# Kernel optimization log

Hardware: AMD Instinct MI355X
Metric: run time of the kernel (lower is better)

## Reference

```python
import jax, jax.numpy as jnp
import numpy as np

B, S, D, H = 2, 2048, 1024, 16
HD = D // H  # head_dim = 64
NEG = -1.0e9


def setup_inputs() -> dict:
    key = jax.random.key(0)
    ks = jax.random.split(key, 9)
    s = 1.0 / np.sqrt(D)
    return {
        "x": jax.random.normal(ks[0], (B, S, D), jnp.float32),
        "mask": jnp.ones((B, S), jnp.float32),
        "Wq": jax.random.normal(ks[1], (D, D), jnp.float32) * s,
        "bq": jnp.zeros((D,), jnp.float32),
        "Wk": jax.random.normal(ks[2], (D, D), jnp.float32) * s,
        "bk": jnp.zeros((D,), jnp.float32),
        "Wv": jax.random.normal(ks[3], (D, D), jnp.float32) * s,
        "bv": jnp.zeros((D,), jnp.float32),
        "Wo": jax.random.normal(ks[4], (D, D), jnp.float32) * s,
        "bo": jnp.zeros((D,), jnp.float32),
    }


def reference(x, mask, Wq, bq, Wk, bk, Wv, bv, Wo, bo):
    # QKV projections -> [B, H, S, HD]
    def proj(t, W, b):
        return (t @ W + b).reshape(B, S, H, HD).transpose(0, 2, 1, 3)

    q = proj(x, Wq, bq)
    k = proj(x, Wk, bk)
    v = proj(x, Wv, bv)

    scores = jnp.einsum("bhqd,bhkd->bhqk", q, k) / jnp.sqrt(jnp.asarray(HD, x.dtype))
    # causal mask: scores * m + (1-m) * -1e9 (matches original exactly)
    cm = jnp.tril(jnp.ones((S, S), x.dtype))[None, None]
    scores = scores * cm + (1.0 - cm) * NEG
    # 2D padding mask branch
    scores = scores + (1.0 - mask[:, None, None, :]) * NEG

    attn = jax.nn.softmax(scores, axis=-1)
    out = jnp.einsum("bhqk,bhkd->bqhd", attn, v).reshape(B, S, D)
    return out @ Wo + bo
```

## Files before the change

kernel.cpp:

```cpp
#include <hip/hip_runtime.h>
#include <cstdint>
#include <cstddef>

typedef __attribute__((ext_vector_type(8))) short short8;
typedef __attribute__((ext_vector_type(4))) float floatx4;
typedef __attribute__((ext_vector_type(4))) unsigned short ushortx4;
typedef __attribute__((ext_vector_type(4))) unsigned int uintx4;

#define MFMA16(a, b, c) __builtin_amdgcn_mfma_f32_16x16x32_bf16((a), (b), (c), 0, 0, 0)

__device__ __forceinline__ unsigned short f2bf(float f) {
  unsigned int u = __builtin_bit_cast(unsigned int, f);
  u += 0x7fffu + ((u >> 16) & 1u);
  return (unsigned short)(u >> 16);
}

typedef __attribute__((address_space(1))) void gvoid_t;
typedef __attribute__((address_space(3))) void svoid_t;
__device__ __forceinline__ void gload_lds16(const void* g, void* l) {
  __builtin_amdgcn_global_load_lds((gvoid_t*)(uintptr_t)g, (svoid_t*)(uintptr_t)l, 16, 0, 0);
}

__global__ void convert_x(const float* __restrict__ x, unsigned short* __restrict__ xb) {
  int i = (blockIdx.x * 256 + threadIdx.x) * 4;
  floatx4 v = *(const floatx4*)(x + i);
  ushortx4 o;
  o[0] = f2bf(v[0]); o[1] = f2bf(v[1]); o[2] = f2bf(v[2]); o[3] = f2bf(v[3]);
  *(ushortx4*)(xb + i) = o;
}

__global__ void transpose_w(const float* __restrict__ Wq, const float* __restrict__ Wk,
                            const float* __restrict__ Wv, const float* __restrict__ Wo,
                            unsigned short* __restrict__ Wqkvt, unsigned short* __restrict__ Wot) {
  __shared__ float tile[32][33];
  int z = blockIdx.z;
  const float* W = (z == 0) ? Wq : (z == 1) ? Wk : (z == 2) ? Wv : Wo;
  unsigned short* out = (z == 3) ? Wot : (Wqkvt + (size_t)z * 1024 * 1024);
  int n0 = blockIdx.x * 32, k0 = blockIdx.y * 32;
  int tx = threadIdx.x, ty = threadIdx.y;
#pragma unroll
  for (int j = 0; j < 4; ++j)
    tile[ty + j * 8][tx] = W[(size_t)(k0 + ty + j * 8) * 1024 + n0 + tx];
  __syncthreads();
#pragma unroll
  for (int j = 0; j < 4; ++j)
    out[(size_t)(n0 + ty + j * 8) * 1024 + k0 + tx] = f2bf(tile[tx][ty + j * 8]);
}

#define GEMM_PROLOGUE()                                                        \
  __shared__ __align__(16) unsigned short As[128 * 64];                        \
  __shared__ __align__(16) unsigned short Bs[128 * 64];                        \
  const int tid = threadIdx.x;                                                 \
  const int lane = tid & 63;                                                   \
  const int wid = tid >> 6;                                                    \
  const int col = lane & 15;                                                   \
  const int quad = lane >> 4;                                                  \
  const int m0 = blockIdx.x * 128;                                             \
  const int n0 = blockIdx.y * 128;                                             \
  const int wm = wid >> 1;                                                     \
  const int wn = wid & 1;                                                      \
  floatx4 acc[4][4];                                                           \
  _Pragma("unroll") for (int i = 0; i < 4; ++i)                                \
      _Pragma("unroll") for (int j = 0; j < 4; ++j)                            \
          acc[i][j] = (floatx4)(0.f);                                          \
  _Pragma("unroll 1") for (int kt = 0; kt < 16; ++kt) {                        \
    __syncthreads();                                                           \
    _Pragma("unroll") for (int call = 0; call < 4; ++call) {                   \
      int c = call * 256 + tid;                                                \
      int r = c >> 3, ch = c & 7;                                              \
      int gk = kt * 64 + ((ch ^ (r & 7)) * 8);                                 \
      gload_lds16(A + (size_t)(m0 + r) * 1024 + gk,                            \
                  As + (size_t)(call * 256 + wid * 64) * 8);                   \
      gload_lds16(Bt + (size_t)(n0 + r) * 1024 + gk,                           \
                  Bs + (size_t)(call * 256 + wid * 64) * 8);                   \
    }                                                                          \
    __syncthreads();                                                           \
    _Pragma("unroll") for (int ks = 0; ks < 2; ++ks) {                         \
      short8 af[4], bf[4];                                                     \
      _Pragma("unroll") for (int rt = 0; rt < 4; ++rt) {                       \
        int row = wm * 64 + rt * 16 + col;                                     \
        af[rt] = *(const short8*)&As[row * 64 + (((ks * 4 + quad) ^ (row & 7)) * 8)]; \
      }                                                                        \
      _Pragma("unroll") for (int ct = 0; ct < 4; ++ct) {                       \
        int row = wn * 64 + ct * 16 + col;                                     \
        bf[ct] = *(const short8*)&Bs[row * 64 + (((ks * 4 + quad) ^ (row & 7)) * 8)]; \
      }                                                                        \
      _Pragma("unroll") for (int rt = 0; rt < 4; ++rt)                         \
          _Pragma("unroll") for (int ct = 0; ct < 4; ++ct)                     \
              acc[rt][ct] = MFMA16(af[rt], bf[ct], acc[rt][ct]);               \
    }                                                                          \
  }

__global__ __launch_bounds__(256)
void gemm_qkv(const unsigned short* __restrict__ A, const unsigned short* __restrict__ Bt,
              const float* __restrict__ bq, const float* __restrict__ bk,
              const float* __restrict__ bv,
              unsigned short* __restrict__ Qo, unsigned short* __restrict__ Ko,
              unsigned short* __restrict__ Vo) {
  GEMM_PROLOGUE()
  const int nseg = n0 >> 10;
  const float* bias = (nseg == 0) ? bq : ((nseg == 1) ? bk : bv);
#pragma unroll
  for (int rt = 0; rt < 4; ++rt) {
#pragma unroll
    for (int ct = 0; ct < 4; ++ct) {
      int mg = m0 + wm * 64 + rt * 16 + quad * 4;
      int ng = n0 + wn * 64 + ct * 16 + col;
      int c = ng & 1023;
      int hh = c >> 6, hd = c & 63;
      int b_ = mg >> 11, s = mg & 2047;
      float bb = bias[c];
      if (nseg == 2) {
        ushortx4 pk;
#pragma unroll
        for (int i = 0; i < 4; ++i) pk[i] = f2bf(acc[rt][ct][i] + bb);
        *(ushortx4*)&Vo[(size_t)(b_ * 16 + hh) * 131072 + (size_t)hd * 2048 + s] = pk;
      } else {
        unsigned short* dst =
            ((nseg == 0) ? Qo : Ko) + ((size_t)(b_ * 16 + hh) * 2048 + s) * 64 + hd;
        float scl = (nseg == 0) ? 0.125f : 1.0f;
#pragma unroll
        for (int i = 0; i < 4; ++i) dst[(size_t)i * 64] = f2bf((acc[rt][ct][i] + bb) * scl);
      }
    }
  }
}

__global__ __launch_bounds__(256)
void gemm_out(const unsigned short* __restrict__ A, const unsigned short* __restrict__ Bt,
              const float* __restrict__ bo, float* __restrict__ Out) {
  GEMM_PROLOGUE()
#pragma unroll
  for (int rt = 0; rt < 4; ++rt) {
#pragma unroll
    for (int ct = 0; ct < 4; ++ct) {
      int mg = m0 + wm * 64 + rt * 16 + quad * 4;
      int ng = n0 + wn * 64 + ct * 16 + col;
      float bb = bo[ng];
#pragma unroll
      for (int i = 0; i < 4; ++i)
        Out[(size_t)(mg + i) * 1024 + ng] = acc[rt][ct][i] + bb;
    }
  }
}

__global__ __launch_bounds__(256, 3)
void flash_attn(const unsigned short* __restrict__ Q, const unsigned short* __restrict__ K,
                const unsigned short* __restrict__ Vt, const float* __restrict__ mask,
                unsigned short* __restrict__ O) {
  __shared__ __align__(16) unsigned short Ks[128 * 64];
  __shared__ __align__(16) unsigned short Vs[64 * 128];
  __shared__ __align__(16) unsigned short Ps[64 * 128];

  const int tid = threadIdx.x;
  const int lane = tid & 63;
  const int wid = tid >> 6;
  const int col = lane & 15;
  const int quad = lane >> 4;
  const int j = 31 - (int)(blockIdx.x >> 5);
  const int bh = blockIdx.x & 31;
  const int b = bh >> 4, h = bh & 15;
  const int q0 = j * 64;
  const int tdiag = j >> 1;

  const unsigned short* Qp = Q + (size_t)bh * 2048 * 64;
  const unsigned short* Kp = K + (size_t)bh * 2048 * 64;
  const unsigned short* Vp = Vt + (size_t)bh * 64 * 2048;
  const float* mp = mask + b * 2048;

  const int lr8 = lane >> 3, lc8 = lane & 7;
  const int lr16 = lane >> 4, lc16 = lane & 15;
  const floatx4 fzero = (floatx4)(0.f);
  const floatx4 fone = (floatx4)(1.f);

#pragma unroll
  for (int i = 0; i < 2; ++i) {
    int seg = wid * 2 + i;
    int r = seg * 8 + lr8;
    gload_lds16(Qp + (size_t)(q0 + r) * 64 + ((lc8 ^ (r & 7)) * 8), Ps + seg * 512);
  }
  __syncthreads();
  short8 qf[2];
  {
    int q = wid * 16 + col;
#pragma unroll
    for (int ks = 0; ks < 2; ++ks)
      qf[ks] = *(const short8*)&Ps[q * 64 + (((ks * 4 + quad) ^ (q & 7)) * 8)];
  }

  floatx4 o[4];
#pragma unroll
  for (int dt = 0; dt < 4; ++dt) o[dt] = fzero;
  float mrow = -1e30f;
  float lrow = 0.f;

#pragma unroll 1
  for (int t = 0; t <= tdiag; ++t) {
    if (t > 0) __syncthreads();
#pragma unroll
    for (int i = 0; i < 4; ++i) {
      int seg = wid * 4 + i;
      int r = seg * 8 + lr8;
      gload_lds16(Kp + (size_t)(t * 128 + r) * 64 + ((lc8 ^ (r & 7)) * 8), Ks + seg * 512);
    }
#pragma unroll
    for (int i = 0; i < 4; ++i) {
      int seg = wid * 4 + i;
      int r = seg * 4 + lr16;
      gload_lds16(Vp + (size_t)r * 2048 + t * 128 + ((lc16 ^ (r & 15)) * 8), Vs + seg * 512);
    }
    __syncthreads();

    floatx4 mbias[8];
#pragma unroll
    for (int rt = 0; rt < 8; ++rt) {
      floatx4 mm = *(const floatx4*)&mp[t * 128 + rt * 16 + quad * 4];
      mbias[rt] = (fone - mm) * -1.0e9f;
    }

    floatx4 sc[8];
#pragma unroll
    for (int rt = 0; rt < 8; ++rt) {
      int kr = rt * 16 + col;
      short8 kf0 = *(const short8*)&Ks[kr * 64 + ((quad ^ (col & 7)) * 8)];
      short8 kf1 = *(const short8*)&Ks[kr * 64 + (((4 + quad) ^ (col & 7)) * 8)];
      floatx4 s0 = MFMA16(kf0, qf[0], fzero);
      s0 = MFMA16(kf1, qf[1], s0);
      sc[rt] = s0 + mbias[rt];
    }
    if (t == tdiag) {
      int qg = q0 + wid * 16 + col;
#pragma unroll
      for (int rt = 0; rt < 8; ++rt)
#pragma unroll
        for (int i = 0; i < 4; ++i)
          if (t * 128 + rt * 16 + quad * 4 + i > qg) sc[rt][i] = -1.0e9f;
    }

    float mt = -1e30f;
#pragma unroll
    for (int rt = 0; rt < 8; ++rt)
      mt = fmaxf(mt, fmaxf(fmaxf(sc[rt][0], sc[rt][1]), fmaxf(sc[rt][2], sc[rt][3])));
    mt = fmaxf(mt, __shfl_xor(mt, 16));
    mt = fmaxf(mt, __shfl_xor(mt, 32));
    float mn = fmaxf(mrow, mt);
    float alpha = __expf(mrow - mn);
    mrow = mn;
    float sum = 0.f;
#pragma unroll
    for (int rt = 0; rt < 8; ++rt)
#pragma unroll
      for (int i = 0; i < 4; ++i) {
        float p = __expf(sc[rt][i] - mn);
        sc[rt][i] = p;
        sum += p;
      }
    sum += __shfl_xor(sum, 16);
    sum += __shfl_xor(sum, 32);
    lrow = lrow * alpha + sum;
#pragma unroll
    for (int dt = 0; dt < 4; ++dt) o[dt] *= alpha;
    {
      int qloc = wid * 16 + col;
#pragma unroll
      for (int rt = 0; rt < 8; ++rt) {
        ushortx4 pk;
#pragma unroll
        for (int i = 0; i < 4; ++i) pk[i] = f2bf(sc[rt][i]);
        int chunk = (rt * 2 + (quad >> 1)) ^ col;
        *(ushortx4*)&Ps[qloc * 128 + chunk * 8 + (quad & 1) * 4] = pk;
      }
    }
#pragma unroll
    for (int ks = 0; ks < 4; ++ks) {
      int ch = ks * 4 + quad;
      short8 pf = *(const short8*)&Ps[(wid * 16 + col) * 128 + ((ch ^ col) * 8)];
#pragma unroll
      for (int dt = 0; dt < 4; ++dt) {
        short8 vf = *(const short8*)&Vs[(dt * 16 + col) * 128 + ((ch ^ col) * 8)];
        o[dt] = MFMA16(vf, pf, o[dt]);
      }
    }
  }

  {
    float inv = 1.0f / lrow;
    int qg = q0 + wid * 16 + col;
    unsigned short* dst = O + ((size_t)(b * 2048 + qg)) * 1024 + h * 64;
#pragma unroll
    for (int dt = 0; dt < 4; ++dt) {
      ushortx4 pk;
#pragma unroll
      for (int i = 0; i < 4; ++i) pk[i] = f2bf(o[dt][i] * inv);
      *(ushortx4*)&dst[dt * 16 + quad * 4] = pk;
    }
  }
}

extern "C" void kernel_launch(void* const* d_in, const int* in_sizes, int n_in,
                              void* d_out, int out_size, void* d_ws, size_t ws_size,
                              hipStream_t stream) {
  (void)in_sizes; (void)n_in; (void)out_size; (void)ws_size;
  const float* x  = (const float*)d_in[0];
  const float* mask = (const float*)d_in[1];
  const float* Wq = (const float*)d_in[2];
  const float* bq = (const float*)d_in[3];
  const float* Wk = (const float*)d_in[4];
  const float* bk = (const float*)d_in[5];
  const float* Wv = (const float*)d_in[6];
  const float* bv = (const float*)d_in[7];
  const float* Wo = (const float*)d_in[8];
  const float* bo = (const float*)d_in[9];
  float* out = (float*)d_out;

  char* ws = (char*)d_ws;
  unsigned short* xb    = (unsigned short*)(ws);
  unsigned short* Wqkvt = (unsigned short*)(ws + (8u << 20));
  unsigned short* Wot   = (unsigned short*)(ws + (14u << 20));
  unsigned short* Qb    = (unsigned short*)(ws + (16u << 20));
  unsigned short* Kb    = (unsigned short*)(ws + (24u << 20));
  unsigned short* Vtb   = (unsigned short*)(ws + (32u << 20));
  unsigned short* Ao    = (unsigned short*)(ws + (40u << 20));

  convert_x<<<4096, 256, 0, stream>>>(x, xb);
  transpose_w<<<dim3(32, 32, 4), dim3(32, 8), 0, stream>>>(Wq, Wk, Wv, Wo, Wqkvt, Wot);
  gemm_qkv<<<dim3(32, 24), 256, 0, stream>>>(xb, Wqkvt, bq, bk, bv, Qb, Kb, Vtb);
  flash_attn<<<dim3(1024), 256, 0, stream>>>(Qb, Kb, Vtb, mask, Ao);
  gemm_out<<<dim3(32, 8), 256, 0, stream>>>(Ao, Wot, bo, out);
}
```

Measured before the change: 197.4 us.

## Shrink GEMM M-tile and attention KV tile to 64 for more occupancy

Both GEMMs move from 128x128 to 64x128 block tiles, which doubles the grid so more workgroups run across the CUs; the output GEMM in particular goes from 256 to 512 blocks. The flash attention kernel switches from 128-wide KV tiles to 64-wide tiles that line up with the 64-row query blocks. This removes the wasted causal work on the diagonal tile and shrinks LDS use. The P buffer now uses a padded row stride instead of an XOR swizzle, and launch bounds are raised to 5 waves per SIMD. The trade-off is less data reuse per tile, more loop iterations with their barriers, and tighter register limits.

Result: slower. 204.7 us (+3.7%).

```diff
diff --git a/kernel.cpp b/kernel.cpp
--- a/kernel.cpp
+++ b/kernel.cpp
@@ -5,7 +5,7 @@
 typedef __attribute__((ext_vector_type(8))) short short8;
 typedef __attribute__((ext_vector_type(4))) float floatx4;
 typedef __attribute__((ext_vector_type(4))) unsigned short ushortx4;
-typedef __attribute__((ext_vector_type(4))) unsigned int uintx4;
+typedef __attribute__((ext_vector_type(2))) unsigned int uintx2;
 
 #define MFMA16(a, b, c) __builtin_amdgcn_mfma_f32_16x16x32_bf16((a), (b), (c), 0, 0, 0)
 
@@ -13,6 +13,10 @@
   unsigned int u = __builtin_bit_cast(unsigned int, f);
   u += 0x7fffu + ((u >> 16) & 1u);
   return (unsigned short)(u >> 16);
+}
+
+__device__ __forceinline__ unsigned int pk_bf16(float a, float b) {
+  return (unsigned int)f2bf(a) | ((unsigned int)f2bf(b) << 16);
 }
 
 typedef __attribute__((address_space(1))) void gvoid_t;
@@ -48,50 +52,53 @@
 }
 
 #define GEMM_PROLOGUE()                                                        \
-  __shared__ __align__(16) unsigned short As[128 * 64];                        \
+  __shared__ __align__(16) unsigned short As[64 * 64];                         \
   __shared__ __align__(16) unsigned short Bs[128 * 64];                        \
   const int tid = threadIdx.x;                                                 \
   const int lane = tid & 63;                                                   \
   const int wid = tid >> 6;                                                    \
   const int col = lane & 15;                                                   \
   const int quad = lane >> 4;                                                  \
-  const int m0 = blockIdx.x * 128;                                             \
+  const int m0 = blockIdx.x * 64;                                              \
   const int n0 = blockIdx.y * 128;                                             \
   const int wm = wid >> 1;                                                     \
   const int wn = wid & 1;                                                      \
-  floatx4 acc[4][4];                                                           \
-  _Pragma("unroll") for (int i = 0; i < 4; ++i)                                \
+  floatx4 acc[2][4];                                                           \
+  _Pragma("unroll") for (int i = 0; i < 2; ++i)                                \
       _Pragma("unroll") for (int j = 0; j < 4; ++j)                            \
           acc[i][j] = (floatx4)(0.f);                                          \
   _Pragma("unroll 1") for (int kt = 0; kt < 16; ++kt) {                        \
     __syncthreads();                                                           \
+    _Pragma("unroll") for (int call = 0; call < 2; ++call) {                   \
+      int c = call * 256 + tid;                                                \
+      int r = c >> 3, ch = c & 7;                                              \
+      gload_lds16(A + (size_t)(m0 + r) * 1024 + kt * 64 + ((ch ^ (r & 7)) * 8),\
+                  As + (size_t)(call * 256 + wid * 64) * 8);                   \
+    }                                                                          \
     _Pragma("unroll") for (int call = 0; call < 4; ++call) {                   \
       int c = call * 256 + tid;                                                \
       int r = c >> 3, ch = c & 7;                                              \
-      int gk = kt * 64 + ((ch ^ (r & 7)) * 8);                                 \
-      gload_lds16(A + (size_t)(m0 + r) * 1024 + gk,                            \
-                  As + (size_t)(call * 256 + wid * 64) * 8);                   \
-      gload_lds16(Bt + (size_t)(n0 + r) * 1024 + gk,                           \
+      gload_lds16(Bt + (size_t)(n0 + r) * 1024 + kt * 64 + ((ch ^ (r & 7)) * 8),\
                   Bs + (size_t)(call * 256 + wid * 64) * 8);                   \
     }                                                                          \
     __syncthreads();                                                           \
     _Pragma("unroll") for (int ks = 0; ks < 2; ++ks) {                         \
-      short8 af[4], bf[4];                                                     \
-      _Pragma("unroll") for (int rt = 0; rt < 4; ++rt) {                       \
-        int row = wm * 64 + rt * 16 + col;                                     \
+      short8 af[2], bf[4];                                                     \
+      _Pragma("unroll") for (int rt = 0; rt < 2; ++rt) {                       \
+        int row = wm * 32 + rt * 16 + col;                                     \
         af[rt] = *(const short8*)&As[row * 64 + (((ks * 4 + quad) ^ (row & 7)) * 8)]; \
       }                                                                        \
       _Pragma("unroll") for (int ct = 0; ct < 4; ++ct) {                       \
         int row = wn * 64 + ct * 16 + col;                                     \
         bf[ct] = *(const short8*)&Bs[row * 64 + (((ks * 4 + quad) ^ (row & 7)) * 8)]; \
       }                                                                        \
-      _Pragma("unroll") for (int rt = 0; rt < 4; ++rt)                         \
+      _Pragma("unroll") for (int rt = 0; rt < 2; ++rt)                         \
           _Pragma("unroll") for (int ct = 0; ct < 4; ++ct)                     \
               acc[rt][ct] = MFMA16(af[rt], bf[ct], acc[rt][ct]);               \
     }                                                                          \
   }
 
-__global__ __launch_bounds__(256)
+__global__ __launch_bounds__(256, 5)
 void gemm_qkv(const unsigned short* __restrict__ A, const unsigned short* __restrict__ Bt,
               const float* __restrict__ bq, const float* __restrict__ bk,
               const float* __restrict__ bv,
@@ -101,10 +108,10 @@
   const int nseg = n0 >> 10;
   const float* bias = (nseg == 0) ? bq : ((nseg == 1) ? bk : bv);
 #pragma unroll
-  for (int rt = 0; rt < 4; ++rt) {
+  for (int rt = 0; rt < 2; ++rt) {
 #pragma unroll
     for (int ct = 0; ct < 4; ++ct) {
-      int mg = m0 + wm * 64 + rt * 16 + quad * 4;
+      int mg = m0 + wm * 32 + rt * 16 + quad * 4;
       int ng = n0 + wn * 64 + ct * 16 + col;
       int c = ng & 1023;
       int hh = c >> 6, hd = c & 63;
@@ -126,15 +133,15 @@
   }
 }
 
-__global__ __launch_bounds__(256)
+__global__ __launch_bounds__(256, 5)
 void gemm_out(const unsigned short* __restrict__ A, const unsigned short* __restrict__ Bt,
               const float* __restrict__ bo, float* __restrict__ Out) {
   GEMM_PROLOGUE()
 #pragma unroll
-  for (int rt = 0; rt < 4; ++rt) {
+  for (int rt = 0; rt < 2; ++rt) {
 #pragma unroll
     for (int ct = 0; ct < 4; ++ct) {
-      int mg = m0 + wm * 64 + rt * 16 + quad * 4;
+      int mg = m0 + wm * 32 + rt * 16 + quad * 4;
       int ng = n0 + wn * 64 + ct * 16 + col;
       float bb = bo[ng];
 #pragma unroll
@@ -144,13 +151,13 @@
   }
 }
 
-__global__ __launch_bounds__(256, 3)
+__global__ __launch_bounds__(256, 5)
 void flash_attn(const unsigned short* __restrict__ Q, const unsigned short* __restrict__ K,
                 const unsigned short* __restrict__ Vt, const float* __restrict__ mask,
                 unsigned short* __restrict__ O) {
-  __shared__ __align__(16) unsigned short Ks[128 * 64];
-  __shared__ __align__(16) unsigned short Vs[64 * 128];
-  __shared__ __align__(16) unsigned short Ps[64 * 128];
+  __shared__ __align__(16) unsigned short Ks[64 * 64];
+  __shared__ __align__(16) unsigned short Vs[64 * 64];
+  __shared__ __align__(16) unsigned short Ps[64 * 72];
 
   const int tid = threadIdx.x;
   const int lane = tid & 63;
@@ -161,23 +168,21 @@
   const int bh = blockIdx.x & 31;
   const int b = bh >> 4, h = bh & 15;
   const int q0 = j * 64;
-  const int tdiag = j >> 1;
+  const int C = j + 1;
 
   const unsigned short* Qp = Q + (size_t)bh * 2048 * 64;
   const unsigned short* Kp = K + (size_t)bh * 2048 * 64;
   const unsigned short* Vp = Vt + (size_t)bh * 64 * 2048;
   const float* mp = mask + b * 2048;
-
-  const int lr8 = lane >> 3, lc8 = lane & 7;
-  const int lr16 = lane >> 4, lc16 = lane & 15;
   const floatx4 fzero = (floatx4)(0.f);
   const floatx4 fone = (floatx4)(1.f);
 
 #pragma unroll
   for (int i = 0; i < 2; ++i) {
-    int seg = wid * 2 + i;
-    int r = seg * 8 + lr8;
-    gload_lds16(Qp + (size_t)(q0 + r) * 64 + ((lc8 ^ (r & 7)) * 8), Ps + seg * 512);
+    int c = i * 256 + tid;
+    int r = c >> 3, ch = c & 7;
+    gload_lds16(Qp + (size_t)(q0 + r) * 64 + ((ch ^ (r & 7)) * 8),
+                Ps + (size_t)(i * 256 + wid * 64) * 8);
   }
   __syncthreads();
   short8 qf[2];
@@ -195,51 +200,54 @@
   float lrow = 0.f;
 
 #pragma unroll 1
-  for (int t = 0; t <= tdiag; ++t) {
+  for (int t = 0; t < C; ++t) {
+    const int kv0 = t * 64;
     if (t > 0) __syncthreads();
 #pragma unroll
-    for (int i = 0; i < 4; ++i) {
-      int seg = wid * 4 + i;
-      int r = seg * 8 + lr8;
-      gload_lds16(Kp + (size_t)(t * 128 + r) * 64 + ((lc8 ^ (r & 7)) * 8), Ks + seg * 512);
-    }
-#pragma unroll
-    for (int i = 0; i < 4; ++i) {
-      int seg = wid * 4 + i;
-      int r = seg * 4 + lr16;
-      gload_lds16(Vp + (size_t)r * 2048 + t * 128 + ((lc16 ^ (r & 15)) * 8), Vs + seg * 512);
+    for (int i = 0; i < 2; ++i) {
+      int c = i * 256 + tid;
+      int r = c >> 3, ch = c & 7;
+      gload_lds16(Kp + (size_t)(kv0 + r) * 64 + ((ch ^ (r & 7)) * 8),
+                  Ks + (size_t)(i * 256 + wid * 64) * 8);
+    }
+#pragma unroll
+    for (int i = 0; i < 2; ++i) {
+      int c = i * 256 + tid;
+      int r = c >> 3, ch = c & 7;
+      gload_lds16(Vp + (size_t)r * 2048 + kv0 + ((ch ^ (r & 7)) * 8),
+                  Vs + (size_t)(i * 256 + wid * 64) * 8);
     }
     __syncthreads();
 
-    floatx4 mbias[8];
-#pragma unroll
-    for (int rt = 0; rt < 8; ++rt) {
-      floatx4 mm = *(const floatx4*)&mp[t * 128 + rt * 16 + quad * 4];
+    floatx4 mbias[4];
+#pragma unroll
+    for (int rt = 0; rt < 4; ++rt) {
+      floatx4 mm = *(const floatx4*)&mp[kv0 + rt * 16 + quad * 4];
       mbias[rt] = (fone - mm) * -1.0e9f;
     }
 
-    floatx4 sc[8];
-#pragma unroll
-    for (int rt = 0; rt < 8; ++rt) {
+    floatx4 sc[4];
+#pragma unroll
+    for (int rt = 0; rt < 4; ++rt) {
       int kr = rt * 16 + col;
-      short8 kf0 = *(const short8*)&Ks[kr * 64 + ((quad ^ (col & 7)) * 8)];
-      short8 kf1 = *(const short8*)&Ks[kr * 64 + (((4 + quad) ^ (col & 7)) * 8)];
+      short8 kf0 = *(const short8*)&Ks[kr * 64 + ((quad ^ (kr & 7)) * 8)];
+      short8 kf1 = *(const short8*)&Ks[kr * 64 + (((4 + quad) ^ (kr & 7)) * 8)];
       floatx4 s0 = MFMA16(kf0, qf[0], fzero);
       s0 = MFMA16(kf1, qf[1], s0);
       sc[rt] = s0 + mbias[rt];
     }
-    if (t == tdiag) {
+    if (t == C - 1) {
       int qg = q0 + wid * 16 + col;
 #pragma unroll
-      for (int rt = 0; rt < 8; ++rt)
+      for (int rt = 0; rt < 4; ++rt)
 #pragma unroll
         for (int i = 0; i < 4; ++i)
-          if (t * 128 + rt * 16 + quad * 4 + i > qg) sc[rt][i] = -1.0e9f;
+          if (kv0 + rt * 16 + quad * 4 + i > qg) sc[rt][i] = -1.0e9f;
     }
 
     float mt = -1e30f;
 #pragma unroll
-    for (int rt = 0; rt < 8; ++rt)
+    for (int rt = 0; rt < 4; ++rt)
       mt = fmaxf(mt, fmaxf(fmaxf(sc[rt][0], sc[rt][1]), fmaxf(sc[rt][2], sc[rt][3])));
     mt = fmaxf(mt, __shfl_xor(mt, 16));
     mt = fmaxf(mt, __shfl_xor(mt, 32));
@@ -248,7 +256,7 @@
     mrow = mn;
     float sum = 0.f;
 #pragma unroll
-    for (int rt = 0; rt < 8; ++rt)
+    for (int rt = 0; rt < 4; ++rt)
 #pragma unroll
       for (int i = 0; i < 4; ++i) {
         float p = __expf(sc[rt][i] - mn);
@@ -260,24 +268,24 @@
     lrow = lrow * alpha + sum;
 #pragma unroll
     for (int dt = 0; dt < 4; ++dt) o[dt] *= alpha;
+
     {
       int qloc = wid * 16 + col;
 #pragma unroll
-      for (int rt = 0; rt < 8; ++rt) {
-        ushortx4 pk;
-#pragma unroll
-        for (int i = 0; i < 4; ++i) pk[i] = f2bf(sc[rt][i]);
-        int chunk = (rt * 2 + (quad >> 1)) ^ col;
-        *(ushortx4*)&Ps[qloc * 128 + chunk * 8 + (quad & 1) * 4] = pk;
+      for (int rt = 0; rt < 4; ++rt) {
+        uintx2 w;
+        w[0] = pk_bf16(sc[rt][0], sc[rt][1]);
+        w[1] = pk_bf16(sc[rt][2], sc[rt][3]);
+        *(uintx2*)&Ps[qloc * 72 + rt * 16 + quad * 4] = w;
       }
     }
 #pragma unroll
-    for (int ks = 0; ks < 4; ++ks) {
-      int ch = ks * 4 + quad;
-      short8 pf = *(const short8*)&Ps[(wid * 16 + col) * 128 + ((ch ^ col) * 8)];
+    for (int ks = 0; ks < 2; ++ks) {
+      short8 pf = *(const short8*)&Ps[(wid * 16 + col) * 72 + ks * 32 + quad * 8];
 #pragma unroll
       for (int dt = 0; dt < 4; ++dt) {
-        short8 vf = *(const short8*)&Vs[(dt * 16 + col) * 128 + ((ch ^ col) * 8)];
+        int vr = dt * 16 + col;
+        short8 vf = *(const short8*)&Vs[vr * 64 + (((ks * 4 + quad) ^ (vr & 7)) * 8)];
         o[dt] = MFMA16(vf, pf, o[dt]);
       }
     }
@@ -324,7 +332,7 @@
 
   convert_x<<<4096, 256, 0, stream>>>(x, xb);
   transpose_w<<<dim3(32, 32, 4), dim3(32, 8), 0, stream>>>(Wq, Wk, Wv, Wo, Wqkvt, Wot);
-  gemm_qkv<<<dim3(32, 24), 256, 0, stream>>>(xb, Wqkvt, bq, bk, bv, Qb, Kb, Vtb);
+  gemm_qkv<<<dim3(64, 24), 256, 0, stream>>>(xb, Wqkvt, bq, bk, bv, Qb, Kb, Vtb);
   flash_attn<<<dim3(1024), 256, 0, stream>>>(Qb, Kb, Vtb, mask, Ao);
-  gemm_out<<<dim3(32, 8), 256, 0, stream>>>(Ao, Wot, bo, out);
-}
+  gemm_out<<<dim3(64, 8), 256, 0, stream>>>(Ao, Wot, bo, out);
+}
```

## Shrink GEMM M-tile to 64 and load Q/K fragments directly from global

Applied to the files above, without the earlier changes.

The GEMM kernels now use 64x128 tiles instead of 128x128, doubling grid size and raising the occupancy hint, to give more blocks for the modest-sized projections. In flash attention, Q and K fragments are read straight from global memory into registers instead of being staged through LDS, which frees the K shared buffer and lets the occupancy hint rise to 4 blocks. The risk is lower data reuse in the GEMMs and uncoalesced, uncached-by-LDS K reads that each wave repeats, adding global traffic and register pressure.

Result: slower. 252.3 us (+27.8%).

```diff
diff --git a/kernel.cpp b/kernel.cpp
--- a/kernel.cpp
+++ b/kernel.cpp
@@ -5,7 +5,6 @@
 typedef __attribute__((ext_vector_type(8))) short short8;
 typedef __attribute__((ext_vector_type(4))) float floatx4;
 typedef __attribute__((ext_vector_type(4))) unsigned short ushortx4;
-typedef __attribute__((ext_vector_type(4))) unsigned int uintx4;
 
 #define MFMA16(a, b, c) __builtin_amdgcn_mfma_f32_16x16x32_bf16((a), (b), (c), 0, 0, 0)
 
@@ -48,50 +47,53 @@
 }
 
 #define GEMM_PROLOGUE()                                                        \
-  __shared__ __align__(16) unsigned short As[128 * 64];                        \
+  __shared__ __align__(16) unsigned short As[64 * 64];                         \
   __shared__ __align__(16) unsigned short Bs[128 * 64];                        \
   const int tid = threadIdx.x;                                                 \
   const int lane = tid & 63;                                                   \
   const int wid = tid >> 6;                                                    \
   const int col = lane & 15;                                                   \
   const int quad = lane >> 4;                                                  \
-  const int m0 = blockIdx.x * 128;                                             \
+  const int m0 = blockIdx.x * 64;                                              \
   const int n0 = blockIdx.y * 128;                                             \
   const int wm = wid >> 1;                                                     \
   const int wn = wid & 1;                                                      \
-  floatx4 acc[4][4];                                                           \
-  _Pragma("unroll") for (int i = 0; i < 4; ++i)                                \
+  floatx4 acc[2][4];                                                           \
+  _Pragma("unroll") for (int i = 0; i < 2; ++i)                                \
       _Pragma("unroll") for (int j = 0; j < 4; ++j)                            \
           acc[i][j] = (floatx4)(0.f);                                          \
   _Pragma("unroll 1") for (int kt = 0; kt < 16; ++kt) {                        \
     __syncthreads();                                                           \
+    _Pragma("unroll") for (int call = 0; call < 2; ++call) {                   \
+      int c = call * 256 + tid;                                                \
+      int r = c >> 3, ch = c & 7;                                              \
+      gload_lds16(A + (size_t)(m0 + r) * 1024 + kt * 64 + ((ch ^ (r & 7)) * 8),\
+                  As + (size_t)(call * 256 + wid * 64) * 8);                   \
+    }                                                                          \
     _Pragma("unroll") for (int call = 0; call < 4; ++call) {                   \
       int c = call * 256 + tid;                                                \
       int r = c >> 3, ch = c & 7;                                              \
-      int gk = kt * 64 + ((ch ^ (r & 7)) * 8);                                 \
-      gload_lds16(A + (size_t)(m0 + r) * 1024 + gk,                            \
-                  As + (size_t)(call * 256 + wid * 64) * 8);                   \
-      gload_lds16(Bt + (size_t)(n0 + r) * 1024 + gk,                           \
+      gload_lds16(Bt + (size_t)(n0 + r) * 1024 + kt * 64 + ((ch ^ (r & 7)) * 8),\
                   Bs + (size_t)(call * 256 + wid * 64) * 8);                   \
     }                                                                          \
     __syncthreads();                                                           \
     _Pragma("unroll") for (int ks = 0; ks < 2; ++ks) {                         \
-      short8 af[4], bf[4];                                                     \
-      _Pragma("unroll") for (int rt = 0; rt < 4; ++rt) {                       \
-        int row = wm * 64 + rt * 16 + col;                                     \
+      short8 af[2], bf[4];                                                     \
+      _Pragma("unroll") for (int rt = 0; rt < 2; ++rt) {                       \
+        int row = wm * 32 + rt * 16 + col;                                     \
         af[rt] = *(const short8*)&As[row * 64 + (((ks * 4 + quad) ^ (row & 7)) * 8)]; \
       }                                                                        \
       _Pragma("unroll") for (int ct = 0; ct < 4; ++ct) {                       \
         int row = wn * 64 + ct * 16 + col;                                     \
         bf[ct] = *(const short8*)&Bs[row * 64 + (((ks * 4 + quad) ^ (row & 7)) * 8)]; \
       }                                                                        \
-      _Pragma("unroll") for (int rt = 0; rt < 4; ++rt)                         \
+      _Pragma("unroll") for (int rt = 0; rt < 2; ++rt)                         \
           _Pragma("unroll") for (int ct = 0; ct < 4; ++ct)                     \
               acc[rt][ct] = MFMA16(af[rt], bf[ct], acc[rt][ct]);               \
     }                                                                          \
   }
 
-__global__ __launch_bounds__(256)
+__global__ __launch_bounds__(256, 5)
 void gemm_qkv(const unsigned short* __restrict__ A, const unsigned short* __restrict__ Bt,
               const float* __restrict__ bq, const float* __restrict__ bk,
               const float* __restrict__ bv,
@@ -101,10 +103,10 @@
   const int nseg = n0 >> 10;
   const float* bias = (nseg == 0) ? bq : ((nseg == 1) ? bk : bv);
 #pragma unroll
-  for (int rt = 0; rt < 4; ++rt) {
+  for (int rt = 0; rt < 2; ++rt) {
 #pragma unroll
     for (int ct = 0; ct < 4; ++ct) {
-      int mg = m0 + wm * 64 + rt * 16 + quad * 4;
+      int mg = m0 + wm * 32 + rt * 16 + quad * 4;
       int ng = n0 + wn * 64 + ct * 16 + col;
       int c = ng & 1023;
       int hh = c >> 6, hd = c & 63;
@@ -126,15 +128,15 @@
   }
 }
 
-__global__ __launch_bounds__(256)
+__global__ __launch_bounds__(256, 5)
 void gemm_out(const unsigned short* __restrict__ A, const unsigned short* __restrict__ Bt,
               const float* __restrict__ bo, float* __restrict__ Out) {
   GEMM_PROLOGUE()
 #pragma unroll
-  for (int rt = 0; rt < 4; ++rt) {
+  for (int rt = 0; rt < 2; ++rt) {
 #pragma unroll
     for (int ct = 0; ct < 4; ++ct) {
-      int mg = m0 + wm * 64 + rt * 16 + quad * 4;
+      int mg = m0 + wm * 32 + rt * 16 + quad * 4;
       int ng = n0 + wn * 64 + ct * 16 + col;
       float bb = bo[ng];
 #pragma unroll
@@ -144,11 +146,10 @@
   }
 }
 
-__global__ __launch_bounds__(256, 3)
+__global__ __launch_bounds__(256, 4)
 void flash_attn(const unsigned short* __restrict__ Q, const unsigned short* __restrict__ K,
                 const unsigned short* __restrict__ Vt, const float* __restrict__ mask,
                 unsigned short* __restrict__ O) {
-  __shared__ __align__(16) unsigned short Ks[128 * 64];
   __shared__ __align__(16) unsigned short Vs[64 * 128];
   __shared__ __align__(16) unsigned short Ps[64 * 128];
 
@@ -167,26 +168,14 @@
   const unsigned short* Kp = K + (size_t)bh * 2048 * 64;
   const unsigned short* Vp = Vt + (size_t)bh * 64 * 2048;
   const float* mp = mask + b * 2048;
-
-  const int lr8 = lane >> 3, lc8 = lane & 7;
   const int lr16 = lane >> 4, lc16 = lane & 15;
   const floatx4 fzero = (floatx4)(0.f);
   const floatx4 fone = (floatx4)(1.f);
 
-#pragma unroll
-  for (int i = 0; i < 2; ++i) {
-    int seg = wid * 2 + i;
-    int r = seg * 8 + lr8;
-    gload_lds16(Qp + (size_t)(q0 + r) * 64 + ((lc8 ^ (r & 7)) * 8), Ps + seg * 512);
-  }
-  __syncthreads();
   short8 qf[2];
-  {
-    int q = wid * 16 + col;
-#pragma unroll
-    for (int ks = 0; ks < 2; ++ks)
-      qf[ks] = *(const short8*)&Ps[q * 64 + (((ks * 4 + quad) ^ (q & 7)) * 8)];
-  }
+#pragma unroll
+  for (int ks = 0; ks < 2; ++ks)
+    qf[ks] = *(const short8*)&Qp[(size_t)(q0 + wid * 16 + col) * 64 + ks * 32 + quad * 8];
 
   floatx4 o[4];
 #pragma unroll
@@ -197,36 +186,31 @@
 #pragma unroll 1
   for (int t = 0; t <= tdiag; ++t) {
     if (t > 0) __syncthreads();
-#pragma unroll
-    for (int i = 0; i < 4; ++i) {
-      int seg = wid * 4 + i;
-      int r = seg * 8 + lr8;
-      gload_lds16(Kp + (size_t)(t * 128 + r) * 64 + ((lc8 ^ (r & 7)) * 8), Ks + seg * 512);
-    }
 #pragma unroll
     for (int i = 0; i < 4; ++i) {
       int seg = wid * 4 + i;
       int r = seg * 4 + lr16;
       gload_lds16(Vp + (size_t)r * 2048 + t * 128 + ((lc16 ^ (r & 15)) * 8), Vs + seg * 512);
     }
+    short8 kf[8][2];
+#pragma unroll
+    for (int rt = 0; rt < 8; ++rt)
+#pragma unroll
+      for (int ks = 0; ks < 2; ++ks)
+        kf[rt][ks] =
+            *(const short8*)&Kp[(size_t)(t * 128 + rt * 16 + col) * 64 + ks * 32 + quad * 8];
     __syncthreads();
 
-    floatx4 mbias[8];
+    floatx4 sc[8];
+#pragma unroll
+    for (int rt = 0; rt < 8; ++rt) {
+      floatx4 s0 = MFMA16(kf[rt][0], qf[0], fzero);
+      sc[rt] = MFMA16(kf[rt][1], qf[1], s0);
+    }
 #pragma unroll
     for (int rt = 0; rt < 8; ++rt) {
       floatx4 mm = *(const floatx4*)&mp[t * 128 + rt * 16 + quad * 4];
-      mbias[rt] = (fone - mm) * -1.0e9f;
-    }
-
-    floatx4 sc[8];
-#pragma unroll
-    for (int rt = 0; rt < 8; ++rt) {
-      int kr = rt * 16 + col;
-      short8 kf0 = *(const short8*)&Ks[kr * 64 + ((quad ^ (col & 7)) * 8)];
-      short8 kf1 = *(const short8*)&Ks[kr * 64 + (((4 + quad) ^ (col & 7)) * 8)];
-      floatx4 s0 = MFMA16(kf0, qf[0], fzero);
-      s0 = MFMA16(kf1, qf[1], s0);
-      sc[rt] = s0 + mbias[rt];
+      sc[rt] += (fone - mm) * -1.0e9f;
     }
     if (t == tdiag) {
       int qg = q0 + wid * 16 + col;
@@ -324,7 +308,7 @@
 
   convert_x<<<4096, 256, 0, stream>>>(x, xb);
   transpose_w<<<dim3(32, 32, 4), dim3(32, 8), 0, stream>>>(Wq, Wk, Wv, Wo, Wqkvt, Wot);
-  gemm_qkv<<<dim3(32, 24), 256, 0, stream>>>(xb, Wqkvt, bq, bk, bv, Qb, Kb, Vtb);
+  gemm_qkv<<<dim3(64, 24), 256, 0, stream>>>(xb, Wqkvt, bq, bk, bv, Qb, Kb, Vtb);
   flash_attn<<<dim3(1024), 256, 0, stream>>>(Qb, Kb, Vtb, mask, Ao);
-  gemm_out<<<dim3(32, 8), 256, 0, stream>>>(Ao, Wot, bo, out);
-}
+  gemm_out<<<dim3(64, 8), 256, 0, stream>>>(Ao, Wot, bo, out);
+}
```
